# Kernel tuning notes

Measured on AMD Instinct MI355X. Metric: run time of the kernel, lower is better.

Reference implementation:

```python
import math
import jax, jax.numpy as jnp
import numpy as np

DIM = 1024
NUM_HEADS = 16
HEAD_DIM = DIM // NUM_HEADS


def setup_inputs() -> dict:
    key = jax.random.key(0)
    ks = jax.random.split(key, 5)
    b, t, d = 2, 2048, DIM
    x = jax.random.normal(ks[0], (b, t, d), dtype=jnp.float32)
    mask = jnp.ones((b, t), dtype=jnp.float32)  # 1 = keep, 0 = pad
    s_in = 1.0 / math.sqrt(d)
    w_qkv = jax.random.normal(ks[1], (3 * d, d), dtype=jnp.float32) * s_in
    b_qkv = jnp.zeros((3 * d,), dtype=jnp.float32)
    w_out = jax.random.normal(ks[2], (d, d), dtype=jnp.float32) * s_in
    b_out = jnp.zeros((d,), dtype=jnp.float32)
    return {"x": x, "mask": mask, "w_qkv": w_qkv, "b_qkv": b_qkv,
            "w_out": w_out, "b_out": b_out}


def reference(x, mask, w_qkv, b_qkv, w_out, b_out):
    b, t, d = x.shape
    h, hd = NUM_HEADS, HEAD_DIM
    # qkv projection (torch Linear: x @ W^T + b)
    qkv = x @ w_qkv.T + b_qkv                          # [b,t,3d]
    q, k, v = jnp.split(qkv, 3, axis=-1)
    def reshape(z):
        return z.reshape(b, t, h, hd).transpose(0, 2, 1, 3)  # [b,h,t,hd]
    q, k, v = reshape(q), reshape(k), reshape(v)
    att = jnp.einsum('bhqd,bhkd->bhqk', q, k) / math.sqrt(hd)  # [b,h,t,t]
    causal = jnp.tril(jnp.ones((t, t), dtype=bool))            # [t,t]
    keep = causal[None, None, :, :] & (mask[:, None, None, :] != 0)
    att = jnp.where(keep, att, -jnp.inf)
    att = jax.nn.softmax(att, axis=-1)
    out = jnp.einsum('bhqk,bhkd->bhqd', att, v)        # [b,h,t,hd]
    out = out.transpose(0, 2, 1, 3).reshape(b, t, d)
    return out @ w_out.T + b_out
```

## Files before the change

### kernel.cpp

```cpp
#include <hip/hip_runtime.h>
#include <cmath>

#define B_ 2
#define T_ 2048
#define D_ 1024
#define H_ 16
#define HD_ 64
#define M_ (B_ * T_)
#define N3_ (3 * D_)
#define K_ 1024

typedef _Float16 halfx8 __attribute__((ext_vector_type(8)));
typedef _Float16 halfx4 __attribute__((ext_vector_type(4)));
typedef float f32x4 __attribute__((ext_vector_type(4)));
typedef float f32x16 __attribute__((ext_vector_type(16)));

#define ASYNC_COPY16(gp, lp) \
  __builtin_amdgcn_global_load_lds((__attribute__((address_space(1))) void*)(gp), \
      (__attribute__((address_space(3))) void*)(lp), 16, 0, 0)

#define QSCALE 0.1803368801111204f

__device__ const int QT_OF[72] = {
    15,15,15,15,15,15,15,15, 14,14,14,14,14,14,14,14,
    13,13,13,13,13,13,13, 12,12,12,12,12,12,12,
    11,11,11,11,11,11, 10,10,10,10,10,10,
    9,9,9,9,9, 8,8,8,8,8, 7,7,7,7, 6,6,6,6,
    5,5,5, 4,4,4, 3,3, 2,2, 1, 0};
__device__ const int C_OF[72] = {
    0,1,2,3,4,5,6,7, 0,1,2,3,4,5,6,7,
    0,1,2,3,4,5,6, 0,1,2,3,4,5,6,
    0,1,2,3,4,5, 0,1,2,3,4,5,
    0,1,2,3,4, 0,1,2,3,4, 0,1,2,3, 0,1,2,3,
    0,1,2, 0,1,2, 0,1, 0,1, 0, 0};
__device__ const int CB_OF[16] = {0,1,2,4,6,9,12,16,20,25,30,36,42,49,56,64};
__device__ const int NC_OF[16] = {1,1,2,2,3,3,4,4,5,5,6,6,7,7,8,8};
#define NSLOT 72
#define NPOSLOT 56

__global__ __launch_bounds__(256) void prep_all(
    const float* __restrict__ x, const float* __restrict__ wq,
    const float* __restrict__ wo, const float* __restrict__ mask,
    _Float16* __restrict__ xh, _Float16* __restrict__ wqh,
    _Float16* __restrict__ woh, float* __restrict__ kbias,
    int* __restrict__ tflags)
{
    int bid = blockIdx.x;
    if (bid >= 4096) {
        int i = (bid - 4096) * 256 + threadIdx.x;
        float mv = mask[i];
        kbias[i] = (mv != 0.f) ? 0.f : -INFINITY;
        unsigned long long bal = __ballot(mv != 0.f);
        if ((threadIdx.x & 63) == 0) tflags[i >> 6] = (bal == ~0ULL) ? 1 : 0;
        return;
    }
    const float* s; _Float16* d; int off;
    if (bid < 2048)      { s = x;  d = xh;  off = bid; }
    else if (bid < 3584) { s = wq; d = wqh; off = bid - 2048; }
    else                 { s = wo; d = woh; off = bid - 3584; }
    int i = (off * 256 + threadIdx.x) * 8;
    float4 a = *(const float4*)(s + i);
    float4 b = *(const float4*)(s + i + 4);
    halfx8 h;
    h[0] = (_Float16)a.x; h[1] = (_Float16)a.y; h[2] = (_Float16)a.z; h[3] = (_Float16)a.w;
    h[4] = (_Float16)b.x; h[5] = (_Float16)b.y; h[6] = (_Float16)b.z; h[7] = (_Float16)b.w;
    *(halfx8*)(d + i) = h;
}

__global__ __launch_bounds__(256) void gemm_qkv(
    const _Float16* __restrict__ A, const _Float16* __restrict__ Wt,
    const float* __restrict__ bias,
    _Float16* __restrict__ qh, _Float16* __restrict__ kh, _Float16* __restrict__ vth)
{
    __shared__ _Float16 As[128 * 32];
    __shared__ _Float16 Bs[128 * 32];
    const int tid = threadIdx.x;
    const int lane = tid & 63, w = tid >> 6;
    const int col = lane & 15, quad = lane >> 4;
    const int wr = w >> 1, wc = w & 1;
    const int m0 = blockIdx.y << 7, n0 = blockIdx.x << 7;

    const int c0 = w * 2, c1 = c0 + 1;
    const int r0 = c0 * 16 + (lane >> 2), r1 = c1 * 16 + (lane >> 2);
    const int ks = (lane & 3) << 3;

    f32x4 acc[4][4] = {};

    for (int k0 = 0; k0 < K_; k0 += 32) {
        ASYNC_COPY16(A  + (size_t)(m0 + r0) * K_ + k0 + ks, &As[c0 * 512]);
        ASYNC_COPY16(A  + (size_t)(m0 + r1) * K_ + k0 + ks, &As[c1 * 512]);
        ASYNC_COPY16(Wt + (size_t)(n0 + r0) * K_ + k0 + ks, &Bs[c0 * 512]);
        ASYNC_COPY16(Wt + (size_t)(n0 + r1) * K_ + k0 + ks, &Bs[c1 * 512]);
        __syncthreads();
        halfx8 af[4], bf[4];
#pragma unroll
        for (int i = 0; i < 4; ++i)
            af[i] = *(const halfx8*)&As[(wr * 64 + i * 16 + col) * 32 + quad * 8];
#pragma unroll
        for (int j = 0; j < 4; ++j)
            bf[j] = *(const halfx8*)&Bs[(wc * 64 + j * 16 + col) * 32 + quad * 8];
#pragma unroll
        for (int i = 0; i < 4; ++i)
#pragma unroll
            for (int j = 0; j < 4; ++j)
                acc[i][j] = __builtin_amdgcn_mfma_f32_16x16x32_f16(af[i], bf[j], acc[i][j], 0, 0, 0);
        __syncthreads();
    }

#pragma unroll
    for (int i = 0; i < 4; ++i) {
#pragma unroll
        for (int r = 0; r < 4; ++r) {
            int m = m0 + wr * 64 + i * 16 + quad * 4 + r;
            int bb = m >> 11, tt = m & (T_ - 1);
#pragma unroll
            for (int j = 0; j < 4; ++j) {
                int n = n0 + wc * 64 + j * 16 + col;
                float val = acc[i][j][r] + bias[n];
                int which = n >> 10, head = (n >> 6) & 15, dd = n & 63;
                if (which == 0) {
                    qh[((size_t)(bb * H_ + head) * T_ + tt) * HD_ + dd] = (_Float16)(val * QSCALE);
                } else if (which == 1) {
                    int hi = ((dd >> 3) ^ (tt & 7) ^ ((tt >> 3) & 7)) & 7;
                    int dds = (hi << 3) | (dd & 7);
                    kh[((size_t)(bb * H_ + head) * T_ + tt) * HD_ + dds] = (_Float16)val;
                } else {
                    int hi = (((tt >> 3) & 7) ^ (dd & 7) ^ ((dd >> 3) & 7)) & 7;
                    int tts = (tt & ~63) | (hi << 3) | (tt & 7);
                    vth[((size_t)(bb * H_ + head) * HD_ + dd) * T_ + tts] = (_Float16)val;
                }
            }
        }
    }
}

__global__ __launch_bounds__(256) void gemm_out(
    const _Float16* __restrict__ A, const _Float16* __restrict__ Wt,
    const float* __restrict__ bias, float* __restrict__ C)
{
    __shared__ _Float16 As[128 * 32];
    __shared__ _Float16 Bs[64 * 32];
    const int tid = threadIdx.x;
    const int lane = tid & 63, w = tid >> 6;
    const int col = lane & 15, quad = lane >> 4;
    const int m0 = blockIdx.y << 7, n0 = blockIdx.x << 6;

    const int c0 = w * 2, c1 = c0 + 1;
    const int rA0 = c0 * 16 + (lane >> 2), rA1 = c1 * 16 + (lane >> 2);
    const int rB = w * 16 + (lane >> 2);
    const int ks = (lane & 3) << 3;

    f32x4 acc[2][4] = {};

    for (int k0 = 0; k0 < K_; k0 += 32) {
        ASYNC_COPY16(A  + (size_t)(m0 + rA0) * K_ + k0 + ks, &As[c0 * 512]);
        ASYNC_COPY16(A  + (size_t)(m0 + rA1) * K_ + k0 + ks, &As[c1 * 512]);
        ASYNC_COPY16(Wt + (size_t)(n0 + rB) * K_ + k0 + ks, &Bs[w * 512]);
        __syncthreads();
        halfx8 af[2], bf[4];
#pragma unroll
        for (int i = 0; i < 2; ++i)
            af[i] = *(const halfx8*)&As[(w * 32 + i * 16 + col) * 32 + quad * 8];
#pragma unroll
        for (int j = 0; j < 4; ++j)
            bf[j] = *(const halfx8*)&Bs[(j * 16 + col) * 32 + quad * 8];
#pragma unroll
        for (int i = 0; i < 2; ++i)
#pragma unroll
            for (int j = 0; j < 4; ++j)
                acc[i][j] = __builtin_amdgcn_mfma_f32_16x16x32_f16(af[i], bf[j], acc[i][j], 0, 0, 0);
        __syncthreads();
    }

#pragma unroll
    for (int i = 0; i < 2; ++i) {
#pragma unroll
        for (int r = 0; r < 4; ++r) {
            int m = m0 + w * 32 + i * 16 + quad * 4 + r;
#pragma unroll
            for (int j = 0; j < 4; ++j) {
                int n = n0 + j * 16 + col;
                C[(size_t)m * D_ + n] = acc[i][j][r] + bias[n];
            }
        }
    }
}

__global__ __launch_bounds__(256) void attn_kernel(
    const _Float16* __restrict__ qh, const _Float16* __restrict__ kh,
    const _Float16* __restrict__ vth, const float* __restrict__ kbias,
    const int* __restrict__ tflags,
    float* __restrict__ pm, float* __restrict__ pl,
    _Float16* __restrict__ po, _Float16* __restrict__ oh)
{
    __shared__ _Float16 Ks[2][64 * 64];
    __shared__ _Float16 Vt[2][64 * 64];

    const int xi = blockIdx.x;
    const int qt = QT_OF[xi], c = C_OF[xi];
    const int h = blockIdx.y, b = blockIdx.z;
    const int tid = threadIdx.x;
    const int lane = tid & 63, w = tid >> 6;
    const int l31 = lane & 31, q2 = lane >> 5;

    const int kt0 = c * 4;
    const int ktend = min(2 * qt + 1, kt0 + 3);

    const int bh = b * H_ + h;
    const _Float16* qp = qh + (size_t)bh * T_ * HD_;
    const _Float16* kp = kh + (size_t)bh * T_ * HD_;
    const _Float16* vp = vth + (size_t)bh * HD_ * T_;
    const float* kb = kbias + (size_t)b * T_;
    const int* tf = tflags + b * 32;

    const int qbase = qt * 128 + w * 32;
    const int q_row = qbase + l31;

    halfx8 bq[4];
#pragma unroll
    for (int hc = 0; hc < 4; ++hc)
        bq[hc] = *(const halfx8*)(qp + (size_t)q_row * HD_ + hc * 16 + q2 * 8);

    float mrow = -INFINITY, lrow = 0.f;
    f32x16 oacc[2] = {};

    {
        const _Float16* ksrc = kp + (size_t)(kt0 * 64 + w * 16) * HD_;
        ASYNC_COPY16(ksrc + lane * 8, &Ks[0][(w * 16) * 64]);
        ASYNC_COPY16(ksrc + 8 * HD_ + lane * 8, &Ks[0][(w * 16 + 8) * 64]);
        const _Float16* vsrc = vp + (size_t)(w * 16 + (lane >> 3)) * T_
                                 + kt0 * 64 + (lane & 7) * 8;
        ASYNC_COPY16(vsrc, &Vt[0][(w * 16) * 64]);
        ASYNC_COPY16(vsrc + 8 * T_, &Vt[0][(w * 16 + 8) * 64]);
    }

    for (int kt = kt0; kt <= ktend; ++kt) {
        const int cur = (kt - kt0) & 1;
        __syncthreads();
        if (kt < ktend) {
            const int nb = cur ^ 1;
            const _Float16* ksrc = kp + (size_t)((kt + 1) * 64 + w * 16) * HD_;
            ASYNC_COPY16(ksrc + lane * 8, &Ks[nb][(w * 16) * 64]);
            ASYNC_COPY16(ksrc + 8 * HD_ + lane * 8, &Ks[nb][(w * 16 + 8) * 64]);
            const _Float16* vsrc = vp + (size_t)(w * 16 + (lane >> 3)) * T_
                                     + (kt + 1) * 64 + (lane & 7) * 8;
            ASYNC_COPY16(vsrc, &Vt[nb][(w * 16) * 64]);
            ASYNC_COPY16(vsrc + 8 * T_, &Vt[nb][(w * 16 + 8) * 64]);
        }
        if (kt * 64 > qbase + 31) continue;

        f32x16 sa[2];
#pragma unroll
        for (int kb2 = 0; kb2 < 2; ++kb2) {
            f32x16 a;
#pragma unroll
            for (int r = 0; r < 16; ++r) a[r] = 0.f;
#pragma unroll
            for (int hc = 0; hc < 4; ++hc) {
                int seg = (hc * 2 + q2) ^ (l31 & 7) ^ ((kb2 * 4 + (l31 >> 3)) & 7);
                halfx8 ka = *(const halfx8*)&Ks[cur][(kb2 * 32 + l31) * 64 + seg * 8];
                a = __builtin_amdgcn_mfma_f32_32x32x16_f16(ka, bq[hc], a, 0, 0, 0);
            }
            sa[kb2] = a;
        }

        float mx = sa[0][0];
#pragma unroll
        for (int r = 1; r < 16; ++r) mx = fmaxf(mx, sa[0][r]);
#pragma unroll
        for (int r = 0; r < 16; ++r) mx = fmaxf(mx, sa[1][r]);
        mx = fmaxf(mx, __shfl_xor(mx, 32, 64));
        float mold = mrow;
        float mnew = fmaxf(mold, mx);
        unsigned long long bump = __ballot(mnew > mold);
        mrow = mnew;

        const bool interior = (kt * 64 + 63 <= qbase);
        const int allkeep = tf[kt];
        halfx4 pf[2][4];
        float rsum = 0.f;
        if (interior && allkeep) {
#pragma unroll
            for (int kb2 = 0; kb2 < 2; ++kb2)
#pragma unroll
                for (int cc = 0; cc < 4; ++cc)
#pragma unroll
                    for (int j = 0; j < 4; ++j) {
                        float pv = exp2f(sa[kb2][cc * 4 + j] - mnew);
                        rsum += pv;
                        pf[kb2][cc][j] = (_Float16)pv;
                    }
        } else {
#pragma unroll
            for (int kb2 = 0; kb2 < 2; ++kb2)
#pragma unroll
                for (int cc = 0; cc < 4; ++cc)
#pragma unroll
                    for (int j = 0; j < 4; ++j) {
                        int key = kt * 64 + kb2 * 32 + j + 8 * cc + 4 * q2;
                        float add = allkeep ? 0.f : kb[key];
                        float pv = (key <= q_row) ? exp2f(sa[kb2][cc * 4 + j] + add - mnew) : 0.f;
                        rsum += pv;
                        pf[kb2][cc][j] = (_Float16)pv;
                    }
        }
        rsum += __shfl_xor(rsum, 32, 64);

        if (bump) {
            float alpha = exp2f(mold - mnew);
            lrow = lrow * alpha + rsum;
#pragma unroll
            for (int db = 0; db < 2; ++db)
#pragma unroll
                for (int r = 0; r < 16; ++r) oacc[db][r] *= alpha;
        } else {
            lrow += rsum;
        }

#pragma unroll
        for (int db = 0; db < 2; ++db)
#pragma unroll
            for (int kb2 = 0; kb2 < 2; ++kb2)
#pragma unroll
                for (int cc = 0; cc < 4; ++cc) {
                    int ck = kb2 * 4 + cc;
                    int seg = ck ^ (l31 & 7) ^ ((db * 4 + (l31 >> 3)) & 7);
                    halfx4 va = *(const halfx4*)&Vt[cur][(db * 32 + l31) * 64 + seg * 8 + q2 * 4];
                    oacc[db] = __builtin_amdgcn_mfma_f32_32x32x8f16(va, pf[kb2][cc], oacc[db], 0, 0, 0);
                }
    }

    const int qloc = w * 32 + l31;
    const int slot = bh * NSLOT + CB_OF[qt] + c;
    if (q2 == 0) {
        pm[(size_t)slot * 128 + qloc] = mrow;
        pl[(size_t)slot * 128 + qloc] = lrow;
    }
    _Float16* pob;
    if (c == 0)
        pob = oh + ((size_t)(b * T_ + qt * 128 + qloc)) * D_ + h * 64;
    else
        pob = po + ((size_t)(bh * NPOSLOT + (CB_OF[qt] - qt) + (c - 1)) * 128 + qloc) * 64;
#pragma unroll
    for (int db = 0; db < 2; ++db)
#pragma unroll
        for (int gg = 0; gg < 4; ++gg) {
            halfx4 ov;
#pragma unroll
            for (int j = 0; j < 4; ++j)
                ov[j] = (_Float16)(oacc[db][gg * 4 + j]);
            *(halfx4*)(pob + db * 32 + 8 * gg + 4 * q2) = ov;
        }
}

__global__ __launch_bounds__(256) void attn_combine(
    const float* __restrict__ pm, const float* __restrict__ pl,
    const _Float16* __restrict__ po, _Float16* __restrict__ oh)
{
    const int qt = blockIdx.x, h = blockIdx.y, b = blockIdx.z;
    const int nc = NC_OF[qt], cb = CB_OF[qt];
    const int bh = b * H_ + h;
    const int tid = threadIdx.x;
    const int r = tid >> 1, dh = tid & 1;

    const int slot0 = bh * NSLOT + cb;
    float mc[8], lc[8];
    float mstar = -INFINITY;
    for (int cc = 0; cc < nc; ++cc) {
        mc[cc] = pm[(size_t)(slot0 + cc) * 128 + r];
        lc[cc] = pl[(size_t)(slot0 + cc) * 128 + r];
        mstar = fmaxf(mstar, mc[cc]);
    }
    float lstar = 0.f, wc[8];
    for (int cc = 0; cc < nc; ++cc) {
        wc[cc] = exp2f(mc[cc] - mstar);
        lstar += wc[cc] * lc[cc];
    }

    _Float16* ohrow = oh + ((size_t)(b * T_ + qt * 128 + r)) * D_ + h * 64 + dh * 32;

    float acc[32];
    {
        float wv = wc[0];
#pragma unroll
        for (int g = 0; g < 4; ++g) {
            halfx8 hv = *(const halfx8*)(ohrow + g * 8);
#pragma unroll
            for (int j = 0; j < 8; ++j)
                acc[g * 8 + j] = wv * (float)hv[j];
        }
    }
    const int pbase = bh * NPOSLOT + (cb - qt);
    for (int cc = 1; cc < nc; ++cc) {
        const _Float16* src = po + ((size_t)(pbase + cc - 1) * 128 + r) * 64 + dh * 32;
        float wv = wc[cc];
#pragma unroll
        for (int g = 0; g < 4; ++g) {
            halfx8 hv = *(const halfx8*)(src + g * 8);
#pragma unroll
            for (int j = 0; j < 8; ++j)
                acc[g * 8 + j] += wv * (float)hv[j];
        }
    }
    float linv = 1.f / lstar;
#pragma unroll
    for (int g = 0; g < 4; ++g) {
        halfx8 ov;
#pragma unroll
        for (int j = 0; j < 8; ++j)
            ov[j] = (_Float16)(acc[g * 8 + j] * linv);
        *(halfx8*)(ohrow + g * 8) = ov;
    }
}

extern "C" void kernel_launch(void* const* d_in, const int* in_sizes, int n_in,
                              void* d_out, int out_size, void* d_ws, size_t ws_size,
                              hipStream_t stream)
{
    (void)in_sizes; (void)n_in; (void)out_size; (void)ws_size;
    const float* x     = (const float*)d_in[0];
    const float* mask  = (const float*)d_in[1];
    const float* w_qkv = (const float*)d_in[2];
    const float* b_qkv = (const float*)d_in[3];
    const float* w_out = (const float*)d_in[4];
    const float* b_out = (const float*)d_in[5];
    float* out = (float*)d_out;

    const size_t QKV1 = (size_t)B_ * H_ * T_ * HD_;
    _Float16* xh  = (_Float16*)d_ws;
    _Float16* wqh = xh  + (size_t)M_ * K_;
    _Float16* woh = wqh + (size_t)N3_ * K_;
    _Float16* qh  = woh + (size_t)D_ * K_;
    _Float16* kh  = qh  + QKV1;
    _Float16* vth = kh  + QKV1;
    _Float16* oh  = vth + QKV1;
    _Float16* po  = oh  + QKV1;
    float* kbias  = (float*)(po + (size_t)32 * NPOSLOT * 128 * 64);
    float* pm     = kbias + (size_t)B_ * T_;
    float* pl     = pm + (size_t)32 * NSLOT * 128;
    int* tflags   = (int*)(pl + (size_t)32 * NSLOT * 128);

    prep_all<<<4112, 256, 0, stream>>>(x, w_qkv, w_out, mask,
                                       xh, wqh, woh, kbias, tflags);
    gemm_qkv<<<dim3(N3_ / 128, M_ / 128), 256, 0, stream>>>(
        xh, wqh, b_qkv, qh, kh, vth);
    attn_kernel<<<dim3(72, H_, B_), 256, 0, stream>>>(
        qh, kh, vth, kbias, tflags, pm, pl, po, oh);
    attn_combine<<<dim3(16, H_, B_), 256, 0, stream>>>(
        pm, pl, po, oh);
    gemm_out<<<dim3(D_ / 64, M_ / 128), 256, 0, stream>>>(
        oh, woh, b_out, out);
}
```

Baseline: 213.3 us.

## Restructure attention softmax with lazy rescaling, per-half-tile processing, and fast exp

The attention inner loop now processes each 32-key half tile separately and skips the upper half when it is fully masked by causality. Rescaling of the running max uses a threshold, so the output accumulator is rescaled only when the new max exceeds the old one by more than a margin. The row sum is reduced across lanes once at the end instead of every tile. The code also switches to the hardware exp2 builtin, packed fp16 conversion with fdot2 summation, s_setprio around the MFMA blocks, and a launch bound of 3 blocks. Lazy rescaling and fdot2 sums of fp16-rounded values can change numerics slightly, and the occupancy hint may cause register spills.

```diff
diff --git a/kernel.cpp b/kernel.cpp
--- a/kernel.cpp
+++ b/kernel.cpp
@@ -12,6 +12,8 @@
 
 typedef _Float16 halfx8 __attribute__((ext_vector_type(8)));
 typedef _Float16 halfx4 __attribute__((ext_vector_type(4)));
+typedef _Float16 halfx2 __attribute__((ext_vector_type(2)));
+typedef __fp16 fp16x2 __attribute__((ext_vector_type(2)));
 typedef float f32x4 __attribute__((ext_vector_type(4)));
 typedef float f32x16 __attribute__((ext_vector_type(16)));
 
@@ -20,6 +22,15 @@
       (__attribute__((address_space(3))) void*)(lp), 16, 0, 0)
 
 #define QSCALE 0.1803368801111204f
+#define RTHR 4.0f
+
+__device__ __forceinline__ float exp2fast(float x) {
+#if __has_builtin(__builtin_amdgcn_exp2f)
+    return __builtin_amdgcn_exp2f(x);
+#else
+    return exp2f(x);
+#endif
+}
 
 __device__ const int QT_OF[72] = {
     15,15,15,15,15,15,15,15, 14,14,14,14,14,14,14,14,
@@ -186,7 +197,7 @@
     }
 }
 
-__global__ __launch_bounds__(256) void attn_kernel(
+__global__ __launch_bounds__(256, 3) void attn_kernel(
     const _Float16* __restrict__ qh, const _Float16* __restrict__ kh,
     const _Float16* __restrict__ vth, const float* __restrict__ kbias,
     const int* __restrict__ tflags,
@@ -221,8 +232,10 @@
     for (int hc = 0; hc < 4; ++hc)
         bq[hc] = *(const halfx8*)(qp + (size_t)q_row * HD_ + hc * 16 + q2 * 8);
 
-    float mrow = -INFINITY, lrow = 0.f;
+    float mrow = -INFINITY;
+    float lrow = 0.f;
     f32x16 oacc[2] = {};
+    const fp16x2 one2 = {(__fp16)1.f, (__fp16)1.f};
 
     {
         const _Float16* ksrc = kp + (size_t)(kt0 * 64 + w * 16) * HD_;
@@ -249,86 +262,101 @@
         }
         if (kt * 64 > qbase + 31) continue;
 
-        f32x16 sa[2];
-#pragma unroll
-        for (int kb2 = 0; kb2 < 2; ++kb2) {
-            f32x16 a;
-#pragma unroll
-            for (int r = 0; r < 16; ++r) a[r] = 0.f;
+        const int allkeep = tf[kt];
+        const int kb2max = (qbase + 31 - kt * 64 >= 32) ? 2 : 1;
+
+        for (int kb2 = 0; kb2 < kb2max; ++kb2) {
+            f32x16 a = {};
+            __builtin_amdgcn_s_setprio(1);
 #pragma unroll
             for (int hc = 0; hc < 4; ++hc) {
                 int seg = (hc * 2 + q2) ^ (l31 & 7) ^ ((kb2 * 4 + (l31 >> 3)) & 7);
                 halfx8 ka = *(const halfx8*)&Ks[cur][(kb2 * 32 + l31) * 64 + seg * 8];
                 a = __builtin_amdgcn_mfma_f32_32x32x16_f16(ka, bq[hc], a, 0, 0, 0);
             }
-            sa[kb2] = a;
-        }
-
-        float mx = sa[0][0];
-#pragma unroll
-        for (int r = 1; r < 16; ++r) mx = fmaxf(mx, sa[0][r]);
-#pragma unroll
-        for (int r = 0; r < 16; ++r) mx = fmaxf(mx, sa[1][r]);
-        mx = fmaxf(mx, __shfl_xor(mx, 32, 64));
-        float mold = mrow;
-        float mnew = fmaxf(mold, mx);
-        unsigned long long bump = __ballot(mnew > mold);
-        mrow = mnew;
-
-        const bool interior = (kt * 64 + 63 <= qbase);
-        const int allkeep = tf[kt];
-        halfx4 pf[2][4];
-        float rsum = 0.f;
-        if (interior && allkeep) {
-#pragma unroll
-            for (int kb2 = 0; kb2 < 2; ++kb2)
-#pragma unroll
-                for (int cc = 0; cc < 4; ++cc)
+            __builtin_amdgcn_s_setprio(0);
+
+            float m8[8];
+#pragma unroll
+            for (int r = 0; r < 8; ++r) m8[r] = fmaxf(a[r], a[r + 8]);
+#pragma unroll
+            for (int r = 0; r < 4; ++r) m8[r] = fmaxf(m8[r], m8[r + 4]);
+            float mx = fmaxf(fmaxf(m8[0], m8[1]), fmaxf(m8[2], m8[3]));
+
+            if (__any(mx > mrow + RTHR)) {
+                float mxo = fmaxf(mx, __shfl_xor(mx, 32, 64));
+                float mnew = fmaxf(mrow, mxo);
+                float alpha = exp2fast(mrow - mnew);
+                lrow *= alpha;
+#pragma unroll
+                for (int db = 0; db < 2; ++db)
+#pragma unroll
+                    for (int r = 0; r < 16; ++r) oacc[db][r] *= alpha;
+                mrow = mnew;
+            }
+
+            const bool fastk = allkeep && (kt * 64 + kb2 * 32 + 31 <= qbase);
+            halfx4 pf[4];
+            float s0 = 0.f, s1 = 0.f;
+            if (fastk) {
+#pragma unroll
+                for (int cc = 0; cc < 4; ++cc) {
+                    float e0 = exp2fast(a[cc * 4 + 0] - mrow);
+                    float e1 = exp2fast(a[cc * 4 + 1] - mrow);
+                    float e2 = exp2fast(a[cc * 4 + 2] - mrow);
+                    float e3 = exp2fast(a[cc * 4 + 3] - mrow);
+                    fp16x2 lo = __builtin_amdgcn_cvt_pkrtz(e0, e1);
+                    fp16x2 hi = __builtin_amdgcn_cvt_pkrtz(e2, e3);
+                    halfx2* pfv = (halfx2*)&pf[cc];
+                    pfv[0] = __builtin_bit_cast(halfx2, lo);
+                    pfv[1] = __builtin_bit_cast(halfx2, hi);
+#if __has_builtin(__builtin_amdgcn_fdot2)
+                    s0 = __builtin_amdgcn_fdot2(lo, one2, s0, false);
+                    s1 = __builtin_amdgcn_fdot2(hi, one2, s1, false);
+#else
+                    s0 += e0 + e1; s1 += e2 + e3;
+#endif
+                }
+            } else {
+#pragma unroll
+                for (int cc = 0; cc < 4; ++cc) {
+                    float e[4];
 #pragma unroll
                     for (int j = 0; j < 4; ++j) {
-                        float pv = exp2f(sa[kb2][cc * 4 + j] - mnew);
-                        rsum += pv;
-                        pf[kb2][cc][j] = (_Float16)pv;
+                        int key = kt * 64 + kb2 * 32 + 8 * cc + 4 * q2 + j;
+                        float add = allkeep ? 0.f : kb[key];
+                        e[j] = (key <= q_row) ? exp2fast(a[cc * 4 + j] + add - mrow) : 0.f;
                     }
-        } else {
-#pragma unroll
-            for (int kb2 = 0; kb2 < 2; ++kb2)
-#pragma unroll
-                for (int cc = 0; cc < 4; ++cc)
-#pragma unroll
-                    for (int j = 0; j < 4; ++j) {
-                        int key = kt * 64 + kb2 * 32 + j + 8 * cc + 4 * q2;
-                        float add = allkeep ? 0.f : kb[key];
-                        float pv = (key <= q_row) ? exp2f(sa[kb2][cc * 4 + j] + add - mnew) : 0.f;
-                        rsum += pv;
-                        pf[kb2][cc][j] = (_Float16)pv;
-                    }
-        }
-        rsum += __shfl_xor(rsum, 32, 64);
-
-        if (bump) {
-            float alpha = exp2f(mold - mnew);
-            lrow = lrow * alpha + rsum;
+                    fp16x2 lo = __builtin_amdgcn_cvt_pkrtz(e[0], e[1]);
+                    fp16x2 hi = __builtin_amdgcn_cvt_pkrtz(e[2], e[3]);
+                    halfx2* pfv = (halfx2*)&pf[cc];
+                    pfv[0] = __builtin_bit_cast(halfx2, lo);
+                    pfv[1] = __builtin_bit_cast(halfx2, hi);
+#if __has_builtin(__builtin_amdgcn_fdot2)
+                    s0 = __builtin_amdgcn_fdot2(lo, one2, s0, false);
+                    s1 = __builtin_amdgcn_fdot2(hi, one2, s1, false);
+#else
+                    s0 += e[0] + e[1]; s1 += e[2] + e[3];
+#endif
+                }
+            }
+            lrow += s0 + s1;
+
+            __builtin_amdgcn_s_setprio(1);
 #pragma unroll
             for (int db = 0; db < 2; ++db)
-#pragma unroll
-                for (int r = 0; r < 16; ++r) oacc[db][r] *= alpha;
-        } else {
-            lrow += rsum;
-        }
-
-#pragma unroll
-        for (int db = 0; db < 2; ++db)
-#pragma unroll
-            for (int kb2 = 0; kb2 < 2; ++kb2)
 #pragma unroll
                 for (int cc = 0; cc < 4; ++cc) {
                     int ck = kb2 * 4 + cc;
                     int seg = ck ^ (l31 & 7) ^ ((db * 4 + (l31 >> 3)) & 7);
                     halfx4 va = *(const halfx4*)&Vt[cur][(db * 32 + l31) * 64 + seg * 8 + q2 * 4];
-                    oacc[db] = __builtin_amdgcn_mfma_f32_32x32x8f16(va, pf[kb2][cc], oacc[db], 0, 0, 0);
+                    oacc[db] = __builtin_amdgcn_mfma_f32_32x32x8f16(va, pf[cc], oacc[db], 0, 0, 0);
                 }
-    }
+            __builtin_amdgcn_s_setprio(0);
+        }
+    }
+
+    lrow += __shfl_xor(lrow, 32, 64);
 
     const int qloc = w * 32 + l31;
     const int slot = bh * NSLOT + CB_OF[qt] + c;
```

New measurement: 196.0 us. 1.09x faster.
